# Optimization experiments

Measured on AMD Instinct MI355X. Metric: run time of the kernel, lower is better.

The kernel has to match this reference:

```python
import jax, jax.numpy as jnp
import numpy as np

B, NPG, H, TD, NF, NL, A = 64, 20, 512, 256, 128, 6, 100
N = B * NPG
E = B * NPG * (NPG - 1)
ANG_LO, ANG_HI = 59.9, 120.1
LOG_MEANS = jnp.array([1.575442910194397, 1.7017393112182617, 1.9781638383865356], jnp.float32)
LOG_STDS = jnp.array([0.24437622725963593, 0.26526379585266113, 0.3535512685775757], jnp.float32)
TWO_PI = 2.0 * np.pi


def _logmap(x, y):
    z = TWO_PI * (y - x)
    return jnp.arctan2(jnp.sin(z), jnp.cos(z)) / TWO_PI


def _lattice_matrix(lengths, angles_deg):
    a = jnp.deg2rad(angles_deg)
    c, s = jnp.cos(a), jnp.sin(a)
    val = jnp.clip((c[:, 0] * c[:, 1] - c[:, 2]) / (s[:, 0] * s[:, 1]), -1.0, 1.0)
    gs = jnp.arccos(val)
    zero = jnp.zeros_like(lengths[:, 0])
    va = jnp.stack([lengths[:, 0] * s[:, 1], zero, lengths[:, 0] * c[:, 1]], 1)
    vb = jnp.stack([-lengths[:, 1] * s[:, 0] * jnp.cos(gs), lengths[:, 1] * s[:, 0] * jnp.sin(gs), lengths[:, 1] * c[:, 0]], 1)
    vc = jnp.stack([zero, zero, lengths[:, 2]], 1)
    return jnp.stack([va, vb, vc], 1)


def _ln(x, g, b, eps=1e-5):
    mu = jnp.mean(x, -1, keepdims=True)
    var = jnp.var(x, -1, keepdims=True)
    return (x - mu) * jax.lax.rsqrt(var + eps) * g + b


def setup_inputs() -> dict:
    key = jax.random.key(0)
    ks = jax.random.split(key, 24)
    # forward data
    t = jax.random.uniform(ks[0], (B, 1), jnp.float32)
    atom_types = jax.random.randint(ks[1], (N,), 1, A + 1, jnp.int32)
    frac_coords = jax.random.uniform(ks[2], (N, 3), jnp.float32)
    lattice_params = 0.5 * jax.random.normal(ks[3], (B, 6), jnp.float32)
    num_atoms = jnp.full((B,), NPG, jnp.int32)
    node2graph = jnp.repeat(jnp.arange(B, dtype=jnp.int32), NPG)
    # fully-connected edges per graph, no self edges (static structure)
    loc = np.arange(NPG)
    src_l, dst_l = np.meshgrid(loc, loc, indexing='ij')
    mask = src_l != dst_l
    src_l, dst_l = src_l[mask], dst_l[mask]  # (NPG*(NPG-1),)
    offs = (np.arange(B)[:, None] * NPG)
    src = (offs + src_l[None, :]).reshape(-1)
    dst = (offs + dst_l[None, :]).reshape(-1)
    edge_index = jnp.asarray(np.stack([src, dst]), jnp.int32)  # (2, E)
    edge2graph = node2graph[edge_index[0]]
    # parameters
    def w(k, shape, fan_in):
        return (jax.random.normal(k, shape, jnp.float32) / np.sqrt(fan_in)).astype(jnp.float32)
    EIN = 3 + 3 * H + 6 + NF * 2 * 3  # 2313
    p = {
        'W_node': w(ks[4], (A, H), A),
        'W_time': w(ks[5], (1, TD), 1),
        'W_latent': w(ks[6], (H + TD, H), H + TD),
        'ln_gamma': jnp.ones((NL, H), jnp.float32),
        'ln_beta': jnp.zeros((NL, H), jnp.float32),
        'We1': w(ks[7], (NL, EIN, H), EIN),
        'be1': jnp.zeros((NL, H), jnp.float32),
        'We2': w(ks[8], (NL, H, H), H),
        'be2': jnp.zeros((NL, H), jnp.float32),
        'Wn1': w(ks[9], (NL, 2 * H, H), 2 * H),
        'bn1': jnp.zeros((NL, H), jnp.float32),
        'Wn2': w(ks[10], (NL, H, H), H),
        'bn2': jnp.zeros((NL, H), jnp.float32),
        'W_numatom': w(ks[11], (NL, A, H), A),
        'fln_gamma': jnp.ones((H,), jnp.float32),
        'fln_beta': jnp.zeros((H,), jnp.float32),
        'W_coord': w(ks[12], (H, 3), H),
        'W_latout': w(ks[13], (2 * H, 6), 2 * H),
        'b_latout': jnp.zeros((6,), jnp.float32),
    }
    return dict(t=t, frac_coords=frac_coords, lattice_params=lattice_params,
                atom_types=atom_types, num_atoms=num_atoms, node2graph=node2graph,
                edge_index=edge_index, edge2graph=edge2graph, **p)


def reference(t, frac_coords, lattice_params, W_node, W_time, W_latent, ln_gamma, ln_beta,
              We1, be1, We2, be2, Wn1, bn1, Wn2, bn2, W_numatom, fln_gamma, fln_beta,
              W_coord, W_latout, b_latout, atom_types, num_atoms, node2graph, edge_index, edge2graph):
    n_nodes = frac_coords.shape[0]
    n_graphs = t.shape[0]
    src, dst = edge_index[0], edge_index[1]
    frac_diff = _logmap(frac_coords[src], frac_coords[dst])  # (E,3)

    atom_oh = jax.nn.one_hot(jnp.clip(atom_types - 1, 0), A, dtype=jnp.float32)
    h = atom_oh @ W_node
    temb = t @ W_time  # (B,TD)
    h = jnp.concatenate([h, temb[node2graph]], -1) @ W_latent

    lattice_flat = lattice_params  # 6-D in directly
    lengths = jnp.exp(lattice_params[:, :3] * LOG_STDS + LOG_MEANS)
    angles_deg = ANG_LO + (ANG_HI - ANG_LO) * jax.nn.sigmoid(lattice_params[:, 3:])
    Lmat = _lattice_matrix(lengths, angles_deg)  # (B,3,3)
    ltl = jnp.einsum('bij,bkj->bik', Lmat, Lmat)  # L @ L^T

    dots = jnp.einsum('eij,ej->ei', ltl[edge2graph], frac_diff)
    unit_dots = dots / (jnp.linalg.norm(dots, axis=-1, keepdims=True) + 1e-12)

    freqs = TWO_PI * jnp.arange(NF, dtype=jnp.float32)
    emb = (frac_diff[..., None] * freqs).reshape(-1, 3 * NF)
    femb = jnp.concatenate([jnp.sin(emb), jnp.cos(emb)], -1)  # (E, 768)

    na_oh = jax.nn.one_hot(num_atoms - 1, A, dtype=jnp.float32)  # (B,100)
    lat_e = lattice_flat[edge2graph]
    counts = jnp.maximum(jax.ops.segment_sum(jnp.ones_like(src, dtype=jnp.float32), src, num_segments=n_nodes), 1.0)[:, None]

    for l in range(NL):
        h_in = h
        hn = _ln(h_in, ln_gamma[l], ln_beta[l])
        na_emb = (na_oh @ W_numatom[l])[edge2graph]
        ef = jnp.concatenate([unit_dots, hn[src], hn[dst], lat_e, femb, na_emb], -1)
        e = jax.nn.silu(jax.nn.silu(ef @ We1[l] + be1[l]) @ We2[l] + be2[l])
        agg = jax.ops.segment_sum(e, src, num_segments=n_nodes) / counts
        out = jax.nn.silu(jax.nn.silu(jnp.concatenate([hn, agg], -1) @ Wn1[l] + bn1[l]) @ Wn2[l] + bn2[l])
        h = h_in + out

    h = _ln(h, fln_gamma, fln_beta)
    pos_v = h @ W_coord  # (N,3)
    sum_pool = jax.ops.segment_sum(h, node2graph, num_segments=n_graphs)
    mean_pool = sum_pool / num_atoms.astype(jnp.float32)[:, None]
    cell_v = jnp.concatenate([mean_pool, sum_pool], -1) @ W_latout + b_latout  # (B,6)
    return pos_v, cell_v
```

## Files before the change

kernel.cpp:

```cpp
#include <hip/hip_runtime.h>
#include <hip/hip_bf16.h>

typedef __hip_bfloat16 bf16;
typedef __attribute__((ext_vector_type(8))) __bf16 bf16x8;
typedef __attribute__((ext_vector_type(4))) float f32x4;

#define B_   64
#define NPG_ 20
#define H_   512
#define TD_  256
#define NF_  128
#define NL_  6
#define A_   100
#define N_   (B_ * NPG_)
#define E_   (B_ * NPG_ * (NPG_-1))
#define EIN_ 2313
#define KF_  832

__device__ __forceinline__ float bf2f(bf16 x) { return __bfloat162float(x); }
__device__ __forceinline__ bf16  f2bf(float x) { return __float2bfloat16(x); }
__device__ __forceinline__ float siluf(float x) { return x / (1.0f + expf(-x)); }
__device__ __forceinline__ float ldf(const void* p, size_t i, int isb) {
    return isb ? bf2f(((const bf16*)p)[i]) : ((const float*)p)[i];
}
__device__ __forceinline__ void async_cp16(const bf16* src, bf16* dst) {
    __builtin_amdgcn_global_load_lds(
        (const __attribute__((address_space(1))) unsigned int*)src,
        (__attribute__((address_space(3))) unsigned int*)dst,
        16, 0, 0);
}

__global__ void detect_dtype(const unsigned int* __restrict__ tw, int* __restrict__ flag) {
    if (threadIdx.x != 0) return;
    int cnt = 0;
    for (int i = 0; i < 32; i++) {
        unsigned b1 = (tw[i] >> 8) & 0xFF;
        if (b1 >= 0x20 && b1 < 0x40) cnt++;
    }
    *flag = (cnt >= 16) ? 1 : 0;
}

__global__ void ws_sentinel(bf16* out) { if (threadIdx.x == 0) out[0] = f2bf(1000.0f); }

__global__ void prep_graph(const void* __restrict__ latp, float* __restrict__ ltl,
                           const int* __restrict__ flag) {
    int b = threadIdx.x;
    if (b >= B_) return;
    int isb = *flag;
    const float LM[3] = {1.575442910194397f, 1.7017393112182617f, 1.9781638383865356f};
    const float LS[3] = {0.24437622725963593f, 0.26526379585266113f, 0.3535512685775757f};
    float lp[6];
    for (int i = 0; i < 6; i++) lp[i] = ldf(latp, b*6 + i, isb);
    float len[3], c[3], s[3];
    for (int i = 0; i < 3; i++) len[i] = expf(lp[i] * LS[i] + LM[i]);
    for (int i = 0; i < 3; i++) {
        float sig = 1.0f / (1.0f + expf(-lp[3+i]));
        float deg = 59.9f + 60.2f * sig;
        float a = deg * 0.017453292519943295f;
        c[i] = cosf(a); s[i] = sinf(a);
    }
    float val = (c[0]*c[1] - c[2]) / (s[0]*s[1]);
    val = fminf(1.0f, fmaxf(-1.0f, val));
    float gs = acosf(val);
    float L[3][3];
    L[0][0] = len[0]*s[1]; L[0][1] = 0.0f;               L[0][2] = len[0]*c[1];
    L[1][0] = -len[1]*s[0]*cosf(gs); L[1][1] = len[1]*s[0]*sinf(gs); L[1][2] = len[1]*c[0];
    L[2][0] = 0.0f; L[2][1] = 0.0f; L[2][2] = len[2];
    for (int i = 0; i < 3; i++)
        for (int k = 0; k < 3; k++)
            ltl[b*9 + i*3 + k] = L[i][0]*L[k][0] + L[i][1]*L[k][1] + L[i][2]*L[k][2];
}

__global__ __launch_bounds__(512) void prep_q(const void* __restrict__ W_time,
                                              const void* __restrict__ W_latent,
                                              float* __restrict__ q,
                                              const int* __restrict__ flag) {
    int j = threadIdx.x;
    int isb = *flag;
    float s0 = 0.0f, s1 = 0.0f, s2 = 0.0f, s3 = 0.0f;
    for (int d = 0; d < TD_; d += 4) {
        s0 += ldf(W_time, d+0, isb) * ldf(W_latent, (size_t)(H_ + d+0)*H_ + j, isb);
        s1 += ldf(W_time, d+1, isb) * ldf(W_latent, (size_t)(H_ + d+1)*H_ + j, isb);
        s2 += ldf(W_time, d+2, isb) * ldf(W_latent, (size_t)(H_ + d+2)*H_ + j, isb);
        s3 += ldf(W_time, d+3, isb) * ldf(W_latent, (size_t)(H_ + d+3)*H_ + j, isb);
    }
    q[j] = (s0 + s1) + (s2 + s3);
}

__global__ __launch_bounds__(256) void pq_gather(const void* __restrict__ W_node,
                                                 const void* __restrict__ W_numatom,
                                                 bf16* __restrict__ PQa,
                                                 const int* __restrict__ flag) {
    int z = blockIdx.x, ch = blockIdx.y;
    int isb = *flag;
    int base = ch * 4096;
    for (int idx = base + threadIdx.x; idx < base + 4096; idx += 256) {
        int r = idx >> 9, c = idx & 511;
        float v = 0.0f;
        if (r < A_) {
            if (z == 0) v = ldf(W_node, (size_t)r*512 + c, isb);
            else        v = ldf(W_numatom, ((size_t)(z-1)*A_ + r)*512 + c, isb);
        }
        PQa[(size_t)z*65536 + idx] = f2bf(v);
    }
}

__global__ __launch_bounds__(256) void transpose_pq(const void* __restrict__ W_latent,
                                                    const void* __restrict__ We1,
                                                    bf16* __restrict__ PQbt,
                                                    const int* __restrict__ flag) {
    __shared__ bf16 tile[32][33];
    int z = blockIdx.z;
    int isb = *flag;
    const void* src = (z == 0) ? W_latent : We1;
    size_t off = (z == 0) ? 0 : ((size_t)(z-1)*EIN_ + 1801)*512;
    bf16* dst = PQbt + (size_t)z*512*512;
    int r0 = blockIdx.y * 32, c0 = blockIdx.x * 32;
    #pragma unroll
    for (int i = 0; i < 32; i += 8)
        tile[threadIdx.y + i][threadIdx.x] =
            f2bf(ldf(src, off + (size_t)(r0 + threadIdx.y + i)*512 + c0 + threadIdx.x, isb));
    __syncthreads();
    #pragma unroll
    for (int i = 0; i < 32; i += 8)
        dst[(size_t)(c0 + threadIdx.y + i)*512 + r0 + threadIdx.x] = tile[threadIdx.x][threadIdx.y + i];
}

__global__ __launch_bounds__(256) void transpose_layer(
    const void* __restrict__ We1p, const void* __restrict__ We2p,
    const void* __restrict__ Wn1p, const void* __restrict__ Wn2p, size_t l,
    bf16* __restrict__ WtAB, bf16* __restrict__ Wtf, bf16* __restrict__ Wte2,
    bf16* __restrict__ Wtn1, bf16* __restrict__ Wtn2,
    const int* __restrict__ flag) {
    __shared__ bf16 tile[32][33];
    int which = blockIdx.z;
    int isb = *flag;
    const void* src; size_t off; bf16* dst; int R; int ldd;
    switch (which) {
        case 0:  src = We1p; off = (l*EIN_ + 3)*512;    dst = WtAB;            R = 512;  ldd = 512;  break;
        case 1:  src = We1p; off = (l*EIN_ + 515)*512;  dst = WtAB + 512*512;  R = 512;  ldd = 512;  break;
        case 2:  src = We1p; off = (l*EIN_ + 1033)*512; dst = Wtf;             R = 768;  ldd = KF_;  break;
        case 3:  src = We2p; off = l*512*512;           dst = Wte2;            R = 512;  ldd = 512;  break;
        case 4:  src = Wn1p; off = l*1024*512;          dst = Wtn1;            R = 1024; ldd = 1024; break;
        default: src = Wn2p; off = l*512*512;           dst = Wtn2;            R = 512;  ldd = 512;  break;
    }
    int r0 = blockIdx.y * 32, c0 = blockIdx.x * 32;
    if (r0 >= R) return;
    #pragma unroll
    for (int i = 0; i < 32; i += 8)
        tile[threadIdx.y + i][threadIdx.x] =
            f2bf(ldf(src, off + (size_t)(r0 + threadIdx.y + i)*512 + c0 + threadIdx.x, isb));
    __syncthreads();
    #pragma unroll
    for (int i = 0; i < 32; i += 8)
        dst[(size_t)(c0 + threadIdx.y + i)*ldd + r0 + threadIdx.x] = tile[threadIdx.x][threadIdx.y + i];
}

__global__ __launch_bounds__(512) void wtf_tail(const void* __restrict__ We1, size_t l,
                                                bf16* __restrict__ Wtf,
                                                const int* __restrict__ flag) {
    int n = threadIdx.x;
    int isb = *flag;
    const int rows[9] = {0, 1, 2, 1027, 1028, 1029, 1030, 1031, 1032};
    #pragma unroll
    for (int j = 0; j < 64; j++) {
        float v = (j < 9) ? ldf(We1, (l*EIN_ + rows[j])*512 + n, isb) : 0.0f;
        Wtf[(size_t)n*KF_ + 768 + j] = f2bf(v);
    }
}

__global__ __launch_bounds__(512) void node_embed_fast(const bf16* __restrict__ P,
                                                       const float* __restrict__ q,
                                                       const void* __restrict__ t,
                                                       const int* __restrict__ atom_types,
                                                       const int* __restrict__ node2graph,
                                                       float* __restrict__ h,
                                                       const int* __restrict__ flag) {
    int i = blockIdx.x, j = threadIdx.x;
    int isb = *flag;
    int at = atom_types[i] - 1; if (at < 0) at = 0;
    float pv = (at < A_) ? bf2f(P[(size_t)at*512 + j]) : 0.0f;
    float tv = ldf(t, node2graph[i], isb);
    h[(size_t)i*H_ + j] = pv + tv * q[j];
}

__global__ __launch_bounds__(384) void edge_prep(const void* __restrict__ frac,
                                                 const int* __restrict__ edge_index,
                                                 const int* __restrict__ e2g,
                                                 const void* __restrict__ latp,
                                                 const int* __restrict__ num_atoms,
                                                 const float* __restrict__ ltl,
                                                 int* __restrict__ edat,
                                                 bf16* __restrict__ femb,
                                                 const int* __restrict__ flag) {
    const float TWO_PI_F = 6.283185307179586f;
    int e = blockIdx.x;
    int isb = *flag;
    int src = edge_index[e], dst = edge_index[E_ + e];
    int tid = threadIdx.x;
    int d = tid >> 7, k = tid & 127;
    float x = ldf(frac, src*3 + d, isb), y = ldf(frac, dst*3 + d, isb);
    float diff = y - x;
    float fd = diff - rintf(diff);
    float sv, cv;
    sincosf(fd * (TWO_PI_F * (float)k), &sv, &cv);
    femb[(size_t)e*KF_ + d*NF_ + k]       = f2bf(sv);
    femb[(size_t)e*KF_ + 384 + d*NF_ + k] = f2bf(cv);
    if (tid < 64) {
        int g = e2g[e];
        float v = 0.0f;
        if (tid < 3) {
            float f3[3];
            for (int dd = 0; dd < 3; dd++) {
                float df = ldf(frac, dst*3 + dd, isb) - ldf(frac, src*3 + dd, isb);
                f3[dd] = df - rintf(df);
            }
            float dots[3];
            for (int i = 0; i < 3; i++)
                dots[i] = ltl[g*9 + i*3 + 0]*f3[0] + ltl[g*9 + i*3 + 1]*f3[1] + ltl[g*9 + i*3 + 2]*f3[2];
            float nrm = sqrtf(dots[0]*dots[0] + dots[1]*dots[1] + dots[2]*dots[2]);
            v = dots[tid] / (nrm + 1e-12f);
        } else if (tid < 9) {
            v = ldf(latp, g*6 + tid - 3, isb);
        }
        femb[(size_t)e*KF_ + 768 + tid] = f2bf(v);
        if (tid == 0) {
            int na = num_atoms[g] - 1;
            if (na < 0 || na >= A_) na = -1;
            edat[e*4 + 0] = src;
            edat[e*4 + 1] = dst;
            edat[e*4 + 2] = na;
            edat[e*4 + 3] = 0;
        }
    }
}

__device__ __forceinline__ float block_sum_256(float v, float* red) {
    for (int o = 32; o; o >>= 1) v += __shfl_down(v, o);
    int w = threadIdx.x >> 6, lane = threadIdx.x & 63;
    if (lane == 0) red[w] = v;
    __syncthreads();
    float s = red[0] + red[1] + red[2] + red[3];
    __syncthreads();
    return s;
}

__global__ __launch_bounds__(256) void ln_kernel(const float* __restrict__ x,
                                                 const void* __restrict__ gamma,
                                                 const void* __restrict__ beta, size_t goff,
                                                 bf16* __restrict__ cat,
                                                 const int* __restrict__ flag) {
    __shared__ float red[4];
    size_t n = blockIdx.x;
    int tid = threadIdx.x;
    int isb = *flag;
    const float* xr = x + n*H_;
    float v0 = xr[tid], v1 = xr[tid + 256];
    float mu = block_sum_256(v0 + v1, red) * (1.0f/512.0f);
    float d0 = v0 - mu, d1 = v1 - mu;
    float var = block_sum_256(d0*d0 + d1*d1, red) * (1.0f/512.0f);
    float rs = 1.0f / sqrtf(var + 1e-5f);
    cat[n*1024 + tid]       = f2bf(d0*rs*ldf(gamma, goff + tid, isb)       + ldf(beta, goff + tid, isb));
    cat[n*1024 + 256 + tid] = f2bf(d1*rs*ldf(gamma, goff + tid + 256, isb) + ldf(beta, goff + tid + 256, isb));
}

template<int EPI, int TM>
__global__ __launch_bounds__(256) void gemm_bt(
        const bf16* __restrict__ A, int lda,
        const bf16* __restrict__ Bt,
        const void* __restrict__ bias, size_t boff,
        bf16* __restrict__ Cb, float* __restrict__ Cf,
        int K, int N,
        size_t zsA, size_t zsB, size_t zsC,
        const int* __restrict__ flag,
        const bf16* __restrict__ hnAB, const bf16* __restrict__ Qc,
        const int* __restrict__ edat, size_t lidx) {
    constexpr int MT = TM / 32;
    __shared__ __align__(16) bf16 As[TM*64];
    __shared__ __align__(16) bf16 Bs[128*64];
    const int z = blockIdx.z;
    A  += (size_t)z * zsA;
    Bt += (size_t)z * zsB;
    const size_t coff = (size_t)z * zsC;
    const int tid = threadIdx.x;
    const int wave = tid >> 6, lane = tid & 63;
    const int lrow = lane & 15, lq = lane >> 4;
    const size_t m0 = (size_t)blockIdx.y * TM;
    const int n0 = blockIdx.x * 128;
    const int wm = (wave >> 1) * (TM/2), wn = (wave & 1) * 64;
    const int ar = lane >> 3;
    const int gk = (lane & 7) ^ ar;
    f32x4 acc[MT][4] = {};

    for (int k0 = 0; k0 < K; k0 += 64) {
        if (k0) __syncthreads();
        #pragma unroll
        for (int i = 0; i < TM/32; i++) {
            int R = wave*(TM/4) + i*8;
            async_cp16(A + (m0 + R + ar)*lda + k0 + gk*8, As + R*64);
        }
        #pragma unroll
        for (int i = 0; i < 4; i++) {
            int R = wave*32 + i*8;
            async_cp16(Bt + (size_t)(n0 + R + ar)*K + k0 + gk*8, Bs + R*64);
        }
        __syncthreads();
        #pragma unroll
        for (int kk = 0; kk < 2; kk++) {
            bf16x8 af[MT], bfr[4];
            #pragma unroll
            for (int mt = 0; mt < MT; mt++) {
                int r = wm + mt*16 + lrow;
                int p = (kk*4 + lq) ^ (r & 7);
                af[mt] = *(const bf16x8*)(As + r*64 + p*8);
            }
            #pragma unroll
            for (int nt = 0; nt < 4; nt++) {
                int r = wn + nt*16 + lrow;
                int p = (kk*4 + lq) ^ (r & 7);
                bfr[nt] = *(const bf16x8*)(Bs + r*64 + p*8);
            }
            #pragma unroll
            for (int mt = 0; mt < MT; mt++)
                #pragma unroll
                for (int nt = 0; nt < 4; nt++)
                    acc[mt][nt] = __builtin_amdgcn_mfma_f32_16x16x32_bf16(af[mt], bfr[nt], acc[mt][nt], 0, 0, 0);
        }
    }

    if constexpr (EPI == 3) {
        const int isb = *flag;
        float b1v[4];
        #pragma unroll
        for (int nt = 0; nt < 4; nt++)
            b1v[nt] = ldf(bias, boff + n0 + wn + nt*16 + lrow, isb);
        #pragma unroll
        for (int mt = 0; mt < MT; mt++) {
            #pragma unroll
            for (int r = 0; r < 4; r++) {
                size_t e = m0 + wm + mt*16 + lq*4 + r;
                const int4 q = *(const int4*)(edat + e*4);
                int se = q.x, de = q.y, na = q.z;
                #pragma unroll
                for (int nt = 0; nt < 4; nt++) {
                    int col = n0 + wn + nt*16 + lrow;
                    float x = acc[mt][nt][r] + b1v[nt]
                            + bf2f(hnAB[(size_t)se*1024 + col])
                            + bf2f(hnAB[(size_t)de*1024 + 512 + col])
                            + (na >= 0 ? bf2f(Qc[(size_t)(1+lidx)*65536 + (size_t)na*512 + col]) : 0.0f);
                    Cb[e*512 + col] = f2bf(siluf(x));
                }
            }
        }
    } else {
        const int isb = bias ? *flag : 0;
        #pragma unroll
        for (int mt = 0; mt < MT; mt++)
            #pragma unroll
            for (int nt = 0; nt < 4; nt++) {
                int col = n0 + wn + nt*16 + lrow;
                float bv = bias ? ldf(bias, boff + col, isb) : 0.0f;
                #pragma unroll
                for (int r = 0; r < 4; r++) {
                    size_t row = m0 + wm + mt*16 + lq*4 + r;
                    float x = acc[mt][nt][r] + bv;
                    if (EPI == 0)      Cb[coff + row*N + col] = f2bf(x);
                    else if (EPI == 1) Cb[coff + row*N + col] = f2bf(siluf(x));
                    else               Cf[coff + row*N + col] += siluf(x);
                }
            }
    }
}

__global__ __launch_bounds__(256) void seg_mean(const bf16* __restrict__ e2,
                                                bf16* __restrict__ cat) {
    int n = blockIdx.x;
    #pragma unroll
    for (int jj = 0; jj < 2; jj++) {
        int j = threadIdx.x + jj*256;
        const bf16* base = e2 + (size_t)n*19*H_ + j;
        float s = 0.0f;
        #pragma unroll
        for (int i = 0; i < 19; i++) s += bf2f(base[(size_t)i*H_]);
        cat[(size_t)n*1024 + 512 + j] = f2bf(s / 19.0f);
    }
}

__global__ __launch_bounds__(256) void pos_out(const bf16* __restrict__ hln,
                                               const void* __restrict__ W_coord,
                                               void* __restrict__ out,
                                               const int* __restrict__ flag) {
    int wave = threadIdx.x >> 6, lane = threadIdx.x & 63;
    int n = blockIdx.x*4 + wave;
    int isb = *flag;
    float s0 = 0, s1 = 0, s2 = 0;
    for (int k = lane; k < H_; k += 64) {
        float hv = bf2f(hln[(size_t)n*1024 + k]);
        s0 += hv * ldf(W_coord, k*3 + 0, isb);
        s1 += hv * ldf(W_coord, k*3 + 1, isb);
        s2 += hv * ldf(W_coord, k*3 + 2, isb);
    }
    for (int o = 32; o; o >>= 1) {
        s0 += __shfl_down(s0, o); s1 += __shfl_down(s1, o); s2 += __shfl_down(s2, o);
    }
    if (lane == 0) {
        if (isb) { bf16* o = (bf16*)out;  o[n*3] = f2bf(s0); o[n*3+1] = f2bf(s1); o[n*3+2] = f2bf(s2); }
        else     { float* o = (float*)out; o[n*3] = s0; o[n*3+1] = s1; o[n*3+2] = s2; }
    }
}

__global__ __launch_bounds__(512) void cell_out(const bf16* __restrict__ hln,
                                                const void* __restrict__ W_latout,
                                                const void* __restrict__ b_latout,
                                                const int* __restrict__ num_atoms,
                                                void* __restrict__ out,
                                                const int* __restrict__ flag) {
    __shared__ float red[8*6];
    int b = blockIdx.x, j = threadIdx.x;
    int isb = *flag;
    float s = 0.0f;
    for (int i = 0; i < NPG_; i++) s += bf2f(hln[(size_t)(b*NPG_ + i)*1024 + j]);
    float m = s / (float)num_atoms[b];
    float p[6];
    #pragma unroll
    for (int c = 0; c < 6; c++)
        p[c] = m * ldf(W_latout, j*6 + c, isb) + s * ldf(W_latout, (512 + j)*6 + c, isb);
    int w = j >> 6, lane = j & 63;
    #pragma unroll
    for (int c = 0; c < 6; c++) {
        float v = p[c];
        for (int o = 32; o; o >>= 1) v += __shfl_down(v, o);
        if (lane == 0) red[w*6 + c] = v;
    }
    __syncthreads();
    if (j < 6) {
        float v = 0.0f;
        for (int w2 = 0; w2 < 8; w2++) v += red[w2*6 + j];
        float r = v + ldf(b_latout, j, isb);
        if (isb) ((bf16*)out)[N_*3 + b*6 + j] = f2bf(r);
        else     ((float*)out)[N_*3 + b*6 + j] = r;
    }
}

extern "C" void kernel_launch(void* const* d_in, const int* in_sizes, int n_in,
                              void* d_out, int out_size, void* d_ws, size_t ws_size,
                              hipStream_t stream) {
    const void* t          = d_in[0];
    const void* frac       = d_in[1];
    const void* latp       = d_in[2];
    const int*  atom_types = (const int*)d_in[3];
    const int*  num_atoms  = (const int*)d_in[4];
    const int*  node2graph = (const int*)d_in[5];
    const int*  edge_index = (const int*)d_in[6];
    const int*  e2g        = (const int*)d_in[7];
    const void* W_node     = d_in[8];
    const void* W_time     = d_in[9];
    const void* W_latent   = d_in[10];
    const void* ln_gamma   = d_in[11];
    const void* ln_beta    = d_in[12];
    const void* We1        = d_in[13];
    const void* be1        = d_in[14];
    const void* We2        = d_in[15];
    const void* be2        = d_in[16];
    const void* Wn1        = d_in[17];
    const void* bn1        = d_in[18];
    const void* Wn2        = d_in[19];
    const void* bn2        = d_in[20];
    const void* W_numatom  = d_in[21];
    const void* fln_gamma  = d_in[22];
    const void* fln_beta   = d_in[23];
    const void* W_coord    = d_in[24];
    const void* W_latout   = d_in[25];
    const void* b_latout   = d_in[26];

    char* p = (char*)d_ws;
    auto alloc = [&](size_t bytes) { char* r = p; p += (bytes + 255) & ~(size_t)255; return r; };
    int*   flag  = (int*)alloc(4);
    float* ltl   = (float*)alloc((size_t)B_*9*4);
    float* q     = (float*)alloc((size_t)H_*4);
    float* h     = (float*)alloc((size_t)N_*H_*4);
    int*   edat  = (int*)alloc((size_t)E_*4*4);
    bf16* hnAB  = (bf16*)alloc((size_t)N_*1024*2);
    bf16* femb  = (bf16*)alloc((size_t)E_*KF_*2);
    bf16* e1    = (bf16*)alloc((size_t)E_*H_*2);
    bf16* e2    = (bf16*)alloc((size_t)E_*H_*2);
    bf16* cat   = (bf16*)alloc((size_t)N_*1024*2);
    bf16* n1s   = (bf16*)alloc((size_t)N_*H_*2);
    bf16* PQc   = (bf16*)alloc((size_t)7*128*512*2);
    bf16* WtAB  = (bf16*)alloc((size_t)1024*512*2);
    bf16* Wtf   = (bf16*)alloc((size_t)512*KF_*2);
    bf16* Wte2  = (bf16*)alloc((size_t)512*512*2);
    bf16* Wtn1  = (bf16*)alloc((size_t)512*1024*2);
    bf16* Wtn2  = (bf16*)alloc((size_t)512*512*2);
    bf16* PQa   = e1;
    bf16* PQbt  = e2;

    if ((size_t)(p - (char*)d_ws) > ws_size) {
        ws_sentinel<<<1, 64, 0, stream>>>((bf16*)d_out);
        return;
    }

    detect_dtype<<<1, 64, 0, stream>>>((const unsigned int*)t, flag);
    prep_graph<<<1, 64, 0, stream>>>(latp, ltl, flag);
    prep_q<<<1, 512, 0, stream>>>(W_time, W_latent, q, flag);
    pq_gather<<<dim3(7, 16), 256, 0, stream>>>(W_node, W_numatom, PQa, flag);
    transpose_pq<<<dim3(16, 16, 7), dim3(32, 8), 0, stream>>>(W_latent, We1, PQbt, flag);
    gemm_bt<0,128><<<dim3(4, 1, 7), 256, 0, stream>>>(
        PQa, 512, PQbt, nullptr, 0, PQc, nullptr, 512, 512,
        (size_t)128*512, (size_t)512*512, (size_t)128*512,
        flag, nullptr, nullptr, nullptr, 0);
    node_embed_fast<<<N_, 512, 0, stream>>>(PQc, q, t, atom_types, node2graph, h, flag);
    edge_prep<<<E_, 384, 0, stream>>>(frac, edge_index, e2g, latp, num_atoms, ltl, edat, femb, flag);

    for (size_t l = 0; l < NL_; l++) {
        transpose_layer<<<dim3(16, 32, 6), dim3(32, 8), 0, stream>>>(
            We1, We2, Wn1, Wn2, l, WtAB, Wtf, Wte2, Wtn1, Wtn2, flag);
        wtf_tail<<<1, 512, 0, stream>>>(We1, l, Wtf, flag);
        ln_kernel<<<N_, 256, 0, stream>>>(h, ln_gamma, ln_beta, l*H_, cat, flag);
        gemm_bt<0,64><<<dim3(8, N_/64), 256, 0, stream>>>(
            cat, 1024, WtAB, nullptr, 0, hnAB, nullptr, 512, 1024, 0, 0, 0,
            flag, nullptr, nullptr, nullptr, 0);
        gemm_bt<3,64><<<dim3(4, E_/64), 256, 0, stream>>>(
            femb, KF_, Wtf, be1, l*H_, e1, nullptr, KF_, 512, 0, 0, 0,
            flag, hnAB, PQc, edat, l);
        gemm_bt<1,64><<<dim3(4, E_/64), 256, 0, stream>>>(
            e1, 512, Wte2, be2, l*H_, e2, nullptr, 512, 512, 0, 0, 0,
            flag, nullptr, nullptr, nullptr, 0);
        seg_mean<<<N_, 256, 0, stream>>>(e2, cat);
        gemm_bt<1,64><<<dim3(4, N_/64), 256, 0, stream>>>(
            cat, 1024, Wtn1, bn1, l*H_, n1s, nullptr, 1024, 512, 0, 0, 0,
            flag, nullptr, nullptr, nullptr, 0);
        gemm_bt<2,64><<<dim3(4, N_/64), 256, 0, stream>>>(
            n1s, 512, Wtn2, bn2, l*H_, nullptr, h, 512, 512, 0, 0, 0,
            flag, nullptr, nullptr, nullptr, 0);
    }

    ln_kernel<<<N_, 256, 0, stream>>>(h, fln_gamma, fln_beta, 0, cat, flag);
    pos_out<<<N_/4, 256, 0, stream>>>(cat, W_coord, d_out, flag);
    cell_out<<<B_, 512, 0, stream>>>(cat, W_latout, b_latout, num_atoms, d_out, flag);
}
```

Measured before the change: 1.189 ms.

## Use FP8 for Fourier-feature edge GEMM, batch weight transposes, precompute graph bias

The Fourier edge features and their weight slice are now stored as FP8 e4m3 and multiplied by a new dedicated kernel using the fp8 MFMA instruction. This halves the bytes of the largest edge input and uses the higher-rate fp8 matrix path, at some cost in accuracy. When the workspace is large enough, all six layers' weights are transposed in one launch up front instead of once per layer. The per-graph num-atoms embedding plus be1 bias is also precomputed into a table, which simplifies the edge epilogue.

After: 1.057 ms. 11.1% less time.

```diff
diff --git a/kernel.cpp b/kernel.cpp
--- a/kernel.cpp
+++ b/kernel.cpp
@@ -2,6 +2,7 @@
 #include <hip/hip_bf16.h>
 
 typedef __hip_bfloat16 bf16;
+typedef unsigned char u8;
 typedef __attribute__((ext_vector_type(8))) __bf16 bf16x8;
 typedef __attribute__((ext_vector_type(4))) float f32x4;
 
@@ -23,7 +24,27 @@
 __device__ __forceinline__ float ldf(const void* p, size_t i, int isb) {
     return isb ? bf2f(((const bf16*)p)[i]) : ((const float*)p)[i];
 }
-__device__ __forceinline__ void async_cp16(const bf16* src, bf16* dst) {
+__device__ __forceinline__ u8 f2f8(float f) {
+    unsigned s = (__float_as_uint(f) >> 24) & 0x80;
+    float a = fabsf(f);
+    if (!(a == a)) return (u8)0x7F;
+    if (a == 0.0f) return (u8)s;
+    if (a >= 448.0f) return (u8)(s | 0x7E);
+    int e; float m = frexpf(a, &e);
+    int ef = e + 6;
+    unsigned code;
+    if (ef >= 1) {
+        int mant = (int)rintf(m * 16.0f) - 8;
+        if (mant == 8) { mant = 0; ef++; }
+        if (ef > 15) return (u8)(s | 0x7E);
+        code = ((unsigned)ef << 3) | (unsigned)mant;
+    } else {
+        int mant = (int)rintf(ldexpf(a, 9));
+        code = (mant >= 8) ? (1u<<3) : (unsigned)mant;
+    }
+    return (u8)(s | code);
+}
+__device__ __forceinline__ void async_cp16(const void* src, void* dst) {
     __builtin_amdgcn_global_load_lds(
         (const __attribute__((address_space(1))) unsigned int*)src,
         (__attribute__((address_space(3))) unsigned int*)dst,
@@ -128,21 +149,23 @@
 
 __global__ __launch_bounds__(256) void transpose_layer(
     const void* __restrict__ We1p, const void* __restrict__ We2p,
-    const void* __restrict__ Wn1p, const void* __restrict__ Wn2p, size_t l,
-    bf16* __restrict__ WtAB, bf16* __restrict__ Wtf, bf16* __restrict__ Wte2,
+    const void* __restrict__ Wn1p, const void* __restrict__ Wn2p, size_t l0, int allmode,
+    bf16* __restrict__ WtAB, u8* __restrict__ Wtf8, bf16* __restrict__ Wte2,
     bf16* __restrict__ Wtn1, bf16* __restrict__ Wtn2,
     const int* __restrict__ flag) {
     __shared__ bf16 tile[32][33];
-    int which = blockIdx.z;
-    int isb = *flag;
-    const void* src; size_t off; bf16* dst; int R; int ldd;
+    int which = blockIdx.z % 6;
+    size_t lz = blockIdx.z / 6;
+    size_t l = l0 + lz, lw = allmode ? lz : 0;
+    int isb = *flag;
+    const void* src; size_t off; bf16* dst = nullptr; int R; int ldd;
     switch (which) {
-        case 0:  src = We1p; off = (l*EIN_ + 3)*512;    dst = WtAB;            R = 512;  ldd = 512;  break;
-        case 1:  src = We1p; off = (l*EIN_ + 515)*512;  dst = WtAB + 512*512;  R = 512;  ldd = 512;  break;
-        case 2:  src = We1p; off = (l*EIN_ + 1033)*512; dst = Wtf;             R = 768;  ldd = KF_;  break;
-        case 3:  src = We2p; off = l*512*512;           dst = Wte2;            R = 512;  ldd = 512;  break;
-        case 4:  src = Wn1p; off = l*1024*512;          dst = Wtn1;            R = 1024; ldd = 1024; break;
-        default: src = Wn2p; off = l*512*512;           dst = Wtn2;            R = 512;  ldd = 512;  break;
+        case 0:  src = We1p; off = (l*EIN_ + 3)*512;    dst = WtAB + lw*512*1024;            R = 512;  ldd = 512;  break;
+        case 1:  src = We1p; off = (l*EIN_ + 515)*512;  dst = WtAB + lw*512*1024 + 512*512;  R = 512;  ldd = 512;  break;
+        case 2:  src = We1p; off = (l*EIN_ + 1033)*512; R = 768; ldd = KF_; break;
+        case 3:  src = We2p; off = l*512*512;           dst = Wte2 + lw*512*512;             R = 512;  ldd = 512;  break;
+        case 4:  src = Wn1p; off = l*1024*512;          dst = Wtn1 + lw*512*1024;            R = 1024; ldd = 1024; break;
+        default: src = Wn2p; off = l*512*512;           dst = Wtn2 + lw*512*512;             R = 512;  ldd = 512;  break;
     }
     int r0 = blockIdx.y * 32, c0 = blockIdx.x * 32;
     if (r0 >= R) return;
@@ -151,22 +174,45 @@
         tile[threadIdx.y + i][threadIdx.x] =
             f2bf(ldf(src, off + (size_t)(r0 + threadIdx.y + i)*512 + c0 + threadIdx.x, isb));
     __syncthreads();
-    #pragma unroll
-    for (int i = 0; i < 32; i += 8)
-        dst[(size_t)(c0 + threadIdx.y + i)*ldd + r0 + threadIdx.x] = tile[threadIdx.x][threadIdx.y + i];
-}
-
-__global__ __launch_bounds__(512) void wtf_tail(const void* __restrict__ We1, size_t l,
-                                                bf16* __restrict__ Wtf,
+    if (which == 2) {
+        u8* d8 = Wtf8 + lw*(size_t)512*KF_;
+        #pragma unroll
+        for (int i = 0; i < 32; i += 8)
+            d8[(size_t)(c0 + threadIdx.y + i)*KF_ + r0 + threadIdx.x] =
+                f2f8(bf2f(tile[threadIdx.x][threadIdx.y + i]));
+    } else {
+        #pragma unroll
+        for (int i = 0; i < 32; i += 8)
+            dst[(size_t)(c0 + threadIdx.y + i)*ldd + r0 + threadIdx.x] = tile[threadIdx.x][threadIdx.y + i];
+    }
+}
+
+__global__ __launch_bounds__(512) void wtf_tail(const void* __restrict__ We1, size_t l0, int allmode,
+                                                u8* __restrict__ Wtf8,
                                                 const int* __restrict__ flag) {
+    size_t lz = blockIdx.x;
+    size_t l = l0 + lz, lw = allmode ? lz : 0;
     int n = threadIdx.x;
     int isb = *flag;
     const int rows[9] = {0, 1, 2, 1027, 1028, 1029, 1030, 1031, 1032};
+    u8* d8 = Wtf8 + lw*(size_t)512*KF_;
     #pragma unroll
     for (int j = 0; j < 64; j++) {
         float v = (j < 9) ? ldf(We1, (l*EIN_ + rows[j])*512 + n, isb) : 0.0f;
-        Wtf[(size_t)n*KF_ + 768 + j] = f2bf(v);
-    }
+        d8[(size_t)n*KF_ + 768 + j] = f2f8(v);
+    }
+}
+
+__global__ __launch_bounds__(512) void cbias_prep(const bf16* __restrict__ PQc,
+                                                  const void* __restrict__ be1,
+                                                  const int* __restrict__ num_atoms,
+                                                  float* __restrict__ cbias,
+                                                  const int* __restrict__ flag) {
+    int l = blockIdx.x, g = blockIdx.y, j = threadIdx.x;
+    int isb = *flag;
+    int na = num_atoms[g] - 1;
+    float qv = (na >= 0 && na < A_) ? bf2f(PQc[(size_t)(1+l)*65536 + (size_t)na*512 + j]) : 0.0f;
+    cbias[((size_t)l*B_ + g)*512 + j] = ldf(be1, l*512 + j, isb) + qv;
 }
 
 __global__ __launch_bounds__(512) void node_embed_fast(const bf16* __restrict__ P,
@@ -188,10 +234,9 @@
                                                  const int* __restrict__ edge_index,
                                                  const int* __restrict__ e2g,
                                                  const void* __restrict__ latp,
-                                                 const int* __restrict__ num_atoms,
                                                  const float* __restrict__ ltl,
                                                  int* __restrict__ edat,
-                                                 bf16* __restrict__ femb,
+                                                 u8* __restrict__ femb8,
                                                  const int* __restrict__ flag) {
     const float TWO_PI_F = 6.283185307179586f;
     int e = blockIdx.x;
@@ -204,8 +249,8 @@
     float fd = diff - rintf(diff);
     float sv, cv;
     sincosf(fd * (TWO_PI_F * (float)k), &sv, &cv);
-    femb[(size_t)e*KF_ + d*NF_ + k]       = f2bf(sv);
-    femb[(size_t)e*KF_ + 384 + d*NF_ + k] = f2bf(cv);
+    femb8[(size_t)e*KF_ + d*NF_ + k]       = f2f8(sv);
+    femb8[(size_t)e*KF_ + 384 + d*NF_ + k] = f2f8(cv);
     if (tid < 64) {
         int g = e2g[e];
         float v = 0.0f;
@@ -223,13 +268,11 @@
         } else if (tid < 9) {
             v = ldf(latp, g*6 + tid - 3, isb);
         }
-        femb[(size_t)e*KF_ + 768 + tid] = f2bf(v);
+        femb8[(size_t)e*KF_ + 768 + tid] = f2f8(v);
         if (tid == 0) {
-            int na = num_atoms[g] - 1;
-            if (na < 0 || na >= A_) na = -1;
             edat[e*4 + 0] = src;
             edat[e*4 + 1] = dst;
-            edat[e*4 + 2] = na;
+            edat[e*4 + 2] = g;
             edat[e*4 + 3] = 0;
         }
     }
@@ -272,9 +315,7 @@
         bf16* __restrict__ Cb, float* __restrict__ Cf,
         int K, int N,
         size_t zsA, size_t zsB, size_t zsC,
-        const int* __restrict__ flag,
-        const bf16* __restrict__ hnAB, const bf16* __restrict__ Qc,
-        const int* __restrict__ edat, size_t lidx) {
+        const int* __restrict__ flag) {
     constexpr int MT = TM / 32;
     __shared__ __align__(16) bf16 As[TM*64];
     __shared__ __align__(16) bf16 Bs[128*64];
@@ -328,47 +369,96 @@
         }
     }
 
-    if constexpr (EPI == 3) {
-        const int isb = *flag;
-        float b1v[4];
-        #pragma unroll
-        for (int nt = 0; nt < 4; nt++)
-            b1v[nt] = ldf(bias, boff + n0 + wn + nt*16 + lrow, isb);
-        #pragma unroll
-        for (int mt = 0; mt < MT; mt++) {
+    const int isb = bias ? *flag : 0;
+    #pragma unroll
+    for (int mt = 0; mt < MT; mt++)
+        #pragma unroll
+        for (int nt = 0; nt < 4; nt++) {
+            int col = n0 + wn + nt*16 + lrow;
+            float bv = bias ? ldf(bias, boff + col, isb) : 0.0f;
             #pragma unroll
             for (int r = 0; r < 4; r++) {
-                size_t e = m0 + wm + mt*16 + lq*4 + r;
-                const int4 q = *(const int4*)(edat + e*4);
-                int se = q.x, de = q.y, na = q.z;
+                size_t row = m0 + wm + mt*16 + lq*4 + r;
+                float x = acc[mt][nt][r] + bv;
+                if (EPI == 0)      Cb[coff + row*N + col] = f2bf(x);
+                else if (EPI == 1) Cb[coff + row*N + col] = f2bf(siluf(x));
+                else               Cf[coff + row*N + col] += siluf(x);
+            }
+        }
+}
+
+__global__ __launch_bounds__(256) void gemm_fp8_e1(
+        const u8* __restrict__ A,
+        const u8* __restrict__ Bt,
+        const float* __restrict__ cbias_l,
+        const bf16* __restrict__ hnAB,
+        const int* __restrict__ edat,
+        bf16* __restrict__ Cb) {
+    __shared__ __align__(16) u8 As[64*64];
+    __shared__ __align__(16) u8 Bs[128*64];
+    const int tid = threadIdx.x;
+    const int wave = tid >> 6, lane = tid & 63;
+    const int lrow = lane & 15, lq = lane >> 4;
+    const size_t m0 = (size_t)blockIdx.y * 64;
+    const int n0 = blockIdx.x * 128;
+    const int wm = (wave >> 1) * 32, wn = (wave & 1) * 64;
+    const int ar = lane >> 2;
+    const int ac = lane & 3;
+    const int gk = ac ^ (ar & 3);
+    f32x4 acc[2][4] = {};
+
+    for (int k0 = 0; k0 < KF_; k0 += 64) {
+        if (k0) __syncthreads();
+        {
+            int R = wave*16;
+            async_cp16(A + (m0 + R + ar)*KF_ + k0 + gk*16, As + R*64);
+        }
+        #pragma unroll
+        for (int i = 0; i < 2; i++) {
+            int R = wave*32 + i*16;
+            async_cp16(Bt + (size_t)(n0 + R + ar)*KF_ + k0 + gk*16, Bs + R*64);
+        }
+        __syncthreads();
+        #pragma unroll
+        for (int kk = 0; kk < 2; kk++) {
+            long long af[2], bfr[4];
+            #pragma unroll
+            for (int mt = 0; mt < 2; mt++) {
+                int r = wm + mt*16 + lrow;
+                int p = (kk*2 + (lq >> 1)) ^ (r & 3);
+                af[mt] = *(const long long*)(As + r*64 + p*16 + (lq & 1)*8);
+            }
+            #pragma unroll
+            for (int nt = 0; nt < 4; nt++) {
+                int r = wn + nt*16 + lrow;
+                int p = (kk*2 + (lq >> 1)) ^ (r & 3);
+                bfr[nt] = *(const long long*)(Bs + r*64 + p*16 + (lq & 1)*8);
+            }
+            #pragma unroll
+            for (int mt = 0; mt < 2; mt++)
                 #pragma unroll
-                for (int nt = 0; nt < 4; nt++) {
-                    int col = n0 + wn + nt*16 + lrow;
-                    float x = acc[mt][nt][r] + b1v[nt]
-                            + bf2f(hnAB[(size_t)se*1024 + col])
-                            + bf2f(hnAB[(size_t)de*1024 + 512 + col])
-                            + (na >= 0 ? bf2f(Qc[(size_t)(1+lidx)*65536 + (size_t)na*512 + col]) : 0.0f);
-                    Cb[e*512 + col] = f2bf(siluf(x));
-                }
-            }
-        }
-    } else {
-        const int isb = bias ? *flag : 0;
-        #pragma unroll
-        for (int mt = 0; mt < MT; mt++)
+                for (int nt = 0; nt < 4; nt++)
+                    acc[mt][nt] = __builtin_amdgcn_mfma_f32_16x16x32_fp8_fp8(af[mt], bfr[nt], acc[mt][nt], 0, 0, 0);
+        }
+    }
+
+    #pragma unroll
+    for (int mt = 0; mt < 2; mt++) {
+        #pragma unroll
+        for (int r = 0; r < 4; r++) {
+            size_t e = m0 + wm + mt*16 + lq*4 + r;
+            const int4 q = *(const int4*)(edat + e*4);
+            int se = q.x, de = q.y, g = q.z;
             #pragma unroll
             for (int nt = 0; nt < 4; nt++) {
                 int col = n0 + wn + nt*16 + lrow;
-                float bv = bias ? ldf(bias, boff + col, isb) : 0.0f;
-                #pragma unroll
-                for (int r = 0; r < 4; r++) {
-                    size_t row = m0 + wm + mt*16 + lq*4 + r;
-                    float x = acc[mt][nt][r] + bv;
-                    if (EPI == 0)      Cb[coff + row*N + col] = f2bf(x);
-                    else if (EPI == 1) Cb[coff + row*N + col] = f2bf(siluf(x));
-                    else               Cf[coff + row*N + col] += siluf(x);
-                }
+                float x = acc[mt][nt][r]
+                        + cbias_l[(size_t)g*512 + col]
+                        + bf2f(hnAB[(size_t)se*1024 + col])
+                        + bf2f(hnAB[(size_t)de*1024 + 512 + col]);
+                Cb[e*512 + col] = f2bf(siluf(x));
             }
+        }
     }
 }
 
@@ -473,6 +563,15 @@
     const void* W_latout   = d_in[25];
     const void* b_latout   = d_in[26];
 
+    const size_t fixed =
+        256 + ((size_t)B_*9*4 + 255 & ~255ull) + 2048 + (size_t)N_*H_*4 + (size_t)E_*16
+        + (size_t)N_*1024*2 + (size_t)E_*KF_ + (size_t)E_*H_*2*2 + (size_t)N_*1024*2
+        + (size_t)N_*H_*2 + (size_t)7*128*512*2 + (size_t)NL_*B_*512*4 + 8192;
+    const size_t perlayer_w = (size_t)512*1024*2 + (size_t)512*KF_ + (size_t)512*512*2
+                            + (size_t)512*1024*2 + (size_t)512*512*2 + 2048;
+    int allmode = (fixed + 6*perlayer_w <= ws_size) ? 1 : 0;
+    size_t nw = allmode ? 6 : 1;
+
     char* p = (char*)d_ws;
     auto alloc = [&](size_t bytes) { char* r = p; p += (bytes + 255) & ~(size_t)255; return r; };
     int*   flag  = (int*)alloc(4);
@@ -481,17 +580,18 @@
     float* h     = (float*)alloc((size_t)N_*H_*4);
     int*   edat  = (int*)alloc((size_t)E_*4*4);
     bf16* hnAB  = (bf16*)alloc((size_t)N_*1024*2);
-    bf16* femb  = (bf16*)alloc((size_t)E_*KF_*2);
+    u8*   femb8 = (u8*)alloc((size_t)E_*KF_);
     bf16* e1    = (bf16*)alloc((size_t)E_*H_*2);
     bf16* e2    = (bf16*)alloc((size_t)E_*H_*2);
     bf16* cat   = (bf16*)alloc((size_t)N_*1024*2);
     bf16* n1s   = (bf16*)alloc((size_t)N_*H_*2);
     bf16* PQc   = (bf16*)alloc((size_t)7*128*512*2);
-    bf16* WtAB  = (bf16*)alloc((size_t)1024*512*2);
-    bf16* Wtf   = (bf16*)alloc((size_t)512*KF_*2);
-    bf16* Wte2  = (bf16*)alloc((size_t)512*512*2);
-    bf16* Wtn1  = (bf16*)alloc((size_t)512*1024*2);
-    bf16* Wtn2  = (bf16*)alloc((size_t)512*512*2);
+    float* cbias = (float*)alloc((size_t)NL_*B_*512*4);
+    bf16* WtAB  = (bf16*)alloc(nw*(size_t)512*1024*2);
+    u8*   Wtf8  = (u8*)alloc(nw*(size_t)512*KF_);
+    bf16* Wte2  = (bf16*)alloc(nw*(size_t)512*512*2);
+    bf16* Wtn1  = (bf16*)alloc(nw*(size_t)512*1024*2);
+    bf16* Wtn2  = (bf16*)alloc(nw*(size_t)512*512*2);
     bf16* PQa   = e1;
     bf16* PQbt  = e2;
 
@@ -507,32 +607,41 @@
     transpose_pq<<<dim3(16, 16, 7), dim3(32, 8), 0, stream>>>(W_latent, We1, PQbt, flag);
     gemm_bt<0,128><<<dim3(4, 1, 7), 256, 0, stream>>>(
         PQa, 512, PQbt, nullptr, 0, PQc, nullptr, 512, 512,
-        (size_t)128*512, (size_t)512*512, (size_t)128*512,
-        flag, nullptr, nullptr, nullptr, 0);
+        (size_t)128*512, (size_t)512*512, (size_t)128*512, flag);
+    cbias_prep<<<dim3(NL_, B_), 512, 0, stream>>>(PQc, be1, num_atoms, cbias, flag);
     node_embed_fast<<<N_, 512, 0, stream>>>(PQc, q, t, atom_types, node2graph, h, flag);
-    edge_prep<<<E_, 384, 0, stream>>>(frac, edge_index, e2g, latp, num_atoms, ltl, edat, femb, flag);
+    edge_prep<<<E_, 384, 0, stream>>>(frac, edge_index, e2g, latp, ltl, edat, femb8, flag);
+
+    if (allmode) {
+        transpose_layer<<<dim3(16, 32, 36), dim3(32, 8), 0, stream>>>(
+            We1, We2, Wn1, Wn2, 0, 1, WtAB, Wtf8, Wte2, Wtn1, Wtn2, flag);
+        wtf_tail<<<6, 512, 0, stream>>>(We1, 0, 1, Wtf8, flag);
+    }
 
     for (size_t l = 0; l < NL_; l++) {
-        transpose_layer<<<dim3(16, 32, 6), dim3(32, 8), 0, stream>>>(
-            We1, We2, Wn1, Wn2, l, WtAB, Wtf, Wte2, Wtn1, Wtn2, flag);
-        wtf_tail<<<1, 512, 0, stream>>>(We1, l, Wtf, flag);
+        size_t lw = allmode ? l : 0;
+        bf16* WtABl = WtAB + lw*512*1024;
+        u8*   Wtf8l = Wtf8 + lw*(size_t)512*KF_;
+        bf16* Wte2l = Wte2 + lw*512*512;
+        bf16* Wtn1l = Wtn1 + lw*512*1024;
+        bf16* Wtn2l = Wtn2 + lw*512*512;
+        if (!allmode) {
+            transpose_layer<<<dim3(16, 32, 6), dim3(32, 8), 0, stream>>>(
+                We1, We2, Wn1, Wn2, l, 0, WtAB, Wtf8, Wte2, Wtn1, Wtn2, flag);
+            wtf_tail<<<1, 512, 0, stream>>>(We1, l, 0, Wtf8, flag);
+        }
         ln_kernel<<<N_, 256, 0, stream>>>(h, ln_gamma, ln_beta, l*H_, cat, flag);
         gemm_bt<0,64><<<dim3(8, N_/64), 256, 0, stream>>>(
-            cat, 1024, WtAB, nullptr, 0, hnAB, nullptr, 512, 1024, 0, 0, 0,
-            flag, nullptr, nullptr, nullptr, 0);
-        gemm_bt<3,64><<<dim3(4, E_/64), 256, 0, stream>>>(
-            femb, KF_, Wtf, be1, l*H_, e1, nullptr, KF_, 512, 0, 0, 0,
-            flag, hnAB, PQc, edat, l);
+            cat, 1024, WtABl, nullptr, 0, hnAB, nullptr, 512, 1024, 0, 0, 0, flag);
+        gemm_fp8_e1<<<dim3(4, E_/64), 256, 0, stream>>>(
+            femb8, Wtf8l, cbias + l*B_*512, hnAB, edat, e1);
         gemm_bt<1,64><<<dim3(4, E_/64), 256, 0, stream>>>(
-            e1, 512, Wte2, be2, l*H_, e2, nullptr, 512, 512, 0, 0, 0,
-            flag, nullptr, nullptr, nullptr, 0);
+            e1, 512, Wte2l, be2, l*H_, e2, nullptr, 512, 512, 0, 0, 0, flag);
         seg_mean<<<N_, 256, 0, stream>>>(e2, cat);
         gemm_bt<1,64><<<dim3(4, N_/64), 256, 0, stream>>>(
-            cat, 1024, Wtn1, bn1, l*H_, n1s, nullptr, 1024, 512, 0, 0, 0,
-            flag, nullptr, nullptr, nullptr, 0);
+            cat, 1024, Wtn1l, bn1, l*H_, n1s, nullptr, 1024, 512, 0, 0, 0, flag);
         gemm_bt<2,64><<<dim3(4, N_/64), 256, 0, stream>>>(
-            n1s, 512, Wtn2, bn2, l*H_, nullptr, h, 512, 512, 0, 0, 0,
-            flag, nullptr, nullptr, nullptr, 0);
+            n1s, 512, Wtn2l, bn2, l*H_, nullptr, h, 512, 512, 0, 0, 0, flag);
     }
 
     ln_kernel<<<N_, 256, 0, stream>>>(h, fln_gamma, fln_beta, 0, cat, flag);
```
